# Performance work log

Measured on AMD Instinct MI355X. Metric: run time of the kernel, lower is better.

Reference implementation:

```python
import jax, jax.numpy as jnp
import numpy as np


def setup_inputs() -> dict:
    key = jax.random.key(0)
    k1, k2, k3 = jax.random.split(key, 3)
    B, F0, D = 8192, 39, 16
    L = 128
    hash_x = jax.random.normal(k1, (B, F0, D), dtype=jnp.float32)
    W0 = jax.random.normal(k2, (F0 * F0, L), dtype=jnp.float32) * 0.05
    W1 = jax.random.normal(k3, (F0 * (L // 2), L), dtype=jnp.float32) * 0.05
    return {"hash_x": hash_x, "W0": W0, "W1": W1}


def reference(hash_x, W0, W1):
    # CIN (Compressed Interaction Network) with layer sizes [128, 128], no bias.
    x0 = hash_x                      # [B, F0, D]
    B, F0, D = x0.shape
    L = W0.shape[1]                  # 128

    # --- layer 0 ---
    # outer product over fields per embedding dim: [B, D, F0, F0] -> flatten (i,j) row-major
    z0 = jnp.einsum('bid,bjd->bdij', x0, x0).reshape(B, D, F0 * F0)
    # conv1d with kernel width 1 == matmul over flattened field-pair dim
    cur0 = jax.nn.relu(jnp.einsum('bdk,kl->bld', z0, W0))   # [B, L, D]
    next_h, direct0 = jnp.split(cur0, 2, axis=1)            # each [B, L/2, D]

    # --- layer 1 (final) ---
    Fk = next_h.shape[1]                                     # L/2 = 64
    z1 = jnp.einsum('bid,bjd->bdij', x0, next_h).reshape(B, D, F0 * Fk)
    cur1 = jax.nn.relu(jnp.einsum('bdk,kl->bld', z1, W1))   # [B, L, D]

    result = jnp.concatenate([direct0, cur1], axis=1)        # [B, L/2 + L, D]
    return jnp.sum(result, axis=-1)                          # [B, 192]
```

## Files before the change

kernel.cpp:

```cpp
#include <hip/hip_runtime.h>
#include <hip/hip_bf16.h>


using short8 = __attribute__((ext_vector_type(8))) short;
using f32x16 = __attribute__((ext_vector_type(16))) float;

#define VSTR 52
#define V_BYTES (128 * VSTR * 4)
#define HSTR 72
#define H_BYTES (128 * HSTR * 2)
#define SMEM_BYTES (V_BYTES + H_BYTES)

#define NSL0 120
#define NSL1 156
#define NSL  (NSL0 + NSL1)
#define NFRAG (NSL * 4 * 64)

__device__ __forceinline__ unsigned short f2bf(float x) {
  __hip_bfloat16 h = __float2bfloat16(x);
  return __builtin_bit_cast(unsigned short, h);
}
__device__ __forceinline__ unsigned cvt2(float lo, float hi) {
  unsigned r;
  asm("v_cvt_pk_bf16_f32 %0, %1, %2" : "=v"(r) : "v"(lo), "v"(hi));
  return r;
}
__device__ __forceinline__ float bf_lo(unsigned w) {
  return __builtin_bit_cast(float, w << 16);
}
__device__ __forceinline__ float bf_hi(unsigned w) {
  return __builtin_bit_cast(float, w & 0xffff0000u);
}

__global__ void pack_w(const float* __restrict__ W0, const float* __restrict__ W1,
                       short8* __restrict__ wpk) {
  int fid = blockIdx.x * 256 + threadIdx.x;
  if (fid >= NFRAG) return;
  int lane = fid & 63;
  int t2 = fid >> 6;
  int nb = t2 & 3, s = t2 >> 2;
  int n = nb * 32 + (lane & 31);
  int kb = (lane >> 5) * 8;
  short8 frag;
  #pragma unroll
  for (int ii = 0; ii < 8; ii++) {
    float val;
    if (s < NSL0) {
      int k = s * 16 + kb + ii;
      int i = k / 48, j = k - i * 48;
      val = (i < 39 && j < 39) ? W0[(i * 39 + j) * 128 + n] : 0.f;
    } else {
      int k = (s - NSL0) * 16 + kb + ii;
      int i = k >> 6, j = k & 63;
      val = W1[(i * 64 + j) * 128 + n];
    }
    frag[ii] = (short)f2bf(val);
  }
  wpk[fid] = frag;
}

__global__ __launch_bounds__(256, 3) void cin_main(const float* __restrict__ X,
                                                   const short8* __restrict__ wpk,
                                                   float* __restrict__ out) {
  extern __shared__ char smem[];
  float* V          = (float*)smem;
  unsigned short* H = (unsigned short*)(smem + V_BYTES);

  const int t    = threadIdx.x;
  const int lane = t & 63;
  const int w    = t >> 6;
  const int l31  = lane & 31, hi = lane >> 5;
  const int b0   = blockIdx.x * 8;

  const float* xb = X + (size_t)b0 * 624;
  for (int f = t * 4; f < 4992; f += 1024) {
    float4 v4 = *(const float4*)(xb + f);
    int bl = f / 624;
    int rem = f - bl * 624;
    int i = rem >> 4, d0 = rem & 15;
    int r = bl * 16 + d0;
    V[(r + 0) * VSTR + i] = v4.x;
    V[(r + 1) * VSTR + i] = v4.y;
    V[(r + 2) * VSTR + i] = v4.z;
    V[(r + 3) * VSTR + i] = v4.w;
  }
  if (t < 128) {
    #pragma unroll
    for (int c = 39; c < VSTR; c++) V[t * VSTR + c] = 0.f;
  }
  __syncthreads();

  const int row = w * 32 + l31;
  const float* vr          = V + row * VSTR;
  const unsigned short* hr = H + row * HSTR;

  f32x16 acc[4];
  #pragma unroll
  for (int nb = 0; nb < 4; nb++)
    #pragma unroll
    for (int e = 0; e < 16; e++) acc[nb][e] = 0.f;

  short8 bc[4], bn[4];
  #pragma unroll
  for (int nb = 0; nb < 4; nb++) bn[nb] = wpk[nb * 64 + lane];

  #pragma unroll 1
  for (int i40 = 0; i40 < 40; i40++) {
    float vi = vr[i40];
    #pragma unroll
    for (int rr = 0; rr < 3; rr++) {
      int sg = i40 * 3 + rr;
      #pragma unroll
      for (int nb = 0; nb < 4; nb++) {
        bc[nb] = bn[nb];
        bn[nb] = wpk[(sg + 1) * 256 + nb * 64 + lane];
      }
      const float* jp = vr + 16 * rr + 8 * hi;
      float4 lo = *(const float4*)jp;
      float4 h4 = *(const float4*)(jp + 4);
      uint4 pk;
      pk.x = cvt2(vi * lo.x, vi * lo.y);
      pk.y = cvt2(vi * lo.z, vi * lo.w);
      pk.z = cvt2(vi * h4.x, vi * h4.y);
      pk.w = cvt2(vi * h4.z, vi * h4.w);
      short8 a = __builtin_bit_cast(short8, pk);
      #pragma unroll
      for (int nb = 0; nb < 4; nb++)
        acc[nb] = __builtin_amdgcn_mfma_f32_32x32x16_bf16(a, bc[nb], acc[nb], 0, 0, 0);
    }
  }

  #pragma unroll
  for (int nb = 0; nb < 2; nb++)
    #pragma unroll
    for (int r = 0; r < 16; r++) {
      int rt = (r & 3) + 8 * (r >> 2) + 4 * hi;
      H[(w * 32 + rt) * HSTR + nb * 32 + l31] = f2bf(fmaxf(acc[nb][r], 0.f));
    }
  #pragma unroll
  for (int nb = 2; nb < 4; nb++) {
    float s0 = 0.f, s1 = 0.f;
    #pragma unroll
    for (int r = 0; r < 8; r++)  s0 += fmaxf(acc[nb][r], 0.f);
    #pragma unroll
    for (int r = 8; r < 16; r++) s1 += fmaxf(acc[nb][r], 0.f);
    s0 += __shfl_xor(s0, 32);
    s1 += __shfl_xor(s1, 32);
    out[(size_t)(b0 + 2 * w + hi) * 192 + (nb - 2) * 32 + l31] = hi ? s1 : s0;
  }
  __syncthreads();

  #pragma unroll
  for (int nb = 0; nb < 4; nb++)
    #pragma unroll
    for (int e = 0; e < 16; e++) acc[nb][e] = 0.f;

  #pragma unroll 1
  for (int i39 = 0; i39 < 39; i39++) {
    float vi = vr[i39];
    #pragma unroll
    for (int rr = 0; rr < 4; rr++) {
      int sg = NSL0 + i39 * 4 + rr;
      #pragma unroll
      for (int nb = 0; nb < 4; nb++) {
        bc[nb] = bn[nb];
        if (sg + 1 < NSL) bn[nb] = wpk[(sg + 1) * 256 + nb * 64 + lane];
      }
      const unsigned short* jp = hr + 16 * rr + 8 * hi;
      uint4 hw = *(const uint4*)jp;
      uint4 pk;
      pk.x = cvt2(vi * bf_lo(hw.x), vi * bf_hi(hw.x));
      pk.y = cvt2(vi * bf_lo(hw.y), vi * bf_hi(hw.y));
      pk.z = cvt2(vi * bf_lo(hw.z), vi * bf_hi(hw.z));
      pk.w = cvt2(vi * bf_lo(hw.w), vi * bf_hi(hw.w));
      short8 a = __builtin_bit_cast(short8, pk);
      #pragma unroll
      for (int nb = 0; nb < 4; nb++)
        acc[nb] = __builtin_amdgcn_mfma_f32_32x32x16_bf16(a, bc[nb], acc[nb], 0, 0, 0);
    }
  }

  #pragma unroll
  for (int nb = 0; nb < 4; nb++) {
    float s0 = 0.f, s1 = 0.f;
    #pragma unroll
    for (int r = 0; r < 8; r++)  s0 += fmaxf(acc[nb][r], 0.f);
    #pragma unroll
    for (int r = 8; r < 16; r++) s1 += fmaxf(acc[nb][r], 0.f);
    s0 += __shfl_xor(s0, 32);
    s1 += __shfl_xor(s1, 32);
    out[(size_t)(b0 + 2 * w + hi) * 192 + 64 + nb * 32 + l31] = hi ? s1 : s0;
  }
}

extern "C" void kernel_launch(void* const* d_in, const int* in_sizes, int n_in,
                              void* d_out, int out_size, void* d_ws, size_t ws_size,
                              hipStream_t stream) {
  (void)in_sizes; (void)n_in; (void)out_size; (void)ws_size;
  const float* X  = (const float*)d_in[0];
  const float* W0 = (const float*)d_in[1];
  const float* W1 = (const float*)d_in[2];
  float* out = (float*)d_out;
  short8* wpk = (short8*)d_ws;

  pack_w<<<(NFRAG + 255) / 256, 256, 0, stream>>>(W0, W1, wpk);
  cin_main<<<1024, 256, SMEM_BYTES, stream>>>(X, wpk, out);
}
```

Before: 231.1 us.

## Double M-tile per wave and stage weight fragments through LDS with async loads

Each block now handles 16 batch items instead of 8, so every wave computes two 32-row M tiles that share each B fragment. The wave count fetching weights from global memory per output row drops by half. Weight fragments are loaded into double-buffered LDS with global_load_lds, which adds a barrier and a vmcnt wait on every k-step. X is now held in LDS as bf16, and the A operands for each row are preloaded into registers. In exchange the kernel uses more registers, runs at lower occupancy (launch bounds 2) with half as many blocks, and pays a per-step __syncthreads that may serialize the MFMA pipeline.

```diff
diff --git a/kernel.cpp b/kernel.cpp
--- a/kernel.cpp
+++ b/kernel.cpp
@@ -5,16 +5,17 @@
 using short8 = __attribute__((ext_vector_type(8))) short;
 using f32x16 = __attribute__((ext_vector_type(16))) float;
 
-#define VSTR 52
-#define V_BYTES (128 * VSTR * 4)
-#define HSTR 72
-#define H_BYTES (128 * HSTR * 2)
-#define SMEM_BYTES (V_BYTES + H_BYTES)
+#define VS 56
+#define V_BYTES (256 * VS * 2)
+#define HS 72
+#define H_BYTES (256 * HS * 2)
+#define BB_OFF (V_BYTES + H_BYTES)
+#define SMEM_BYTES (BB_OFF + 8192)
 
 #define NSL0 120
 #define NSL1 156
 #define NSL  (NSL0 + NSL1)
-#define NFRAG (NSL * 4 * 64)
+#define NFRAG (NSL * 256)
 
 __device__ __forceinline__ unsigned short f2bf(float x) {
   __hip_bfloat16 h = __float2bfloat16(x);
@@ -30,6 +31,21 @@
 }
 __device__ __forceinline__ float bf_hi(unsigned w) {
   return __builtin_bit_cast(float, w & 0xffff0000u);
+}
+__device__ __forceinline__ float bf2f(unsigned short b) {
+  return __builtin_bit_cast(float, ((unsigned)b) << 16);
+}
+__device__ __forceinline__ short8 mk_a(float vi, uint4 p) {
+  uint4 pk;
+  pk.x = cvt2(vi * bf_lo(p.x), vi * bf_hi(p.x));
+  pk.y = cvt2(vi * bf_lo(p.y), vi * bf_hi(p.y));
+  pk.z = cvt2(vi * bf_lo(p.z), vi * bf_hi(p.z));
+  pk.w = cvt2(vi * bf_lo(p.w), vi * bf_hi(p.w));
+  return __builtin_bit_cast(short8, pk);
+}
+__device__ __forceinline__ void stage16(const void* g, char* l) {
+  __builtin_amdgcn_global_load_lds((const __attribute__((address_space(1))) void*)g,
+                                   (__attribute__((address_space(3))) void*)l, 16, 0, 0);
 }
 
 __global__ void pack_w(const float* __restrict__ W0, const float* __restrict__ W1,
@@ -59,138 +75,168 @@
   wpk[fid] = frag;
 }
 
-__global__ __launch_bounds__(256, 3) void cin_main(const float* __restrict__ X,
+__global__ __launch_bounds__(256, 2) void cin_main(const float* __restrict__ X,
                                                    const short8* __restrict__ wpk,
                                                    float* __restrict__ out) {
   extern __shared__ char smem[];
-  float* V          = (float*)smem;
-  unsigned short* H = (unsigned short*)(smem + V_BYTES);
+  unsigned short* Vb = (unsigned short*)smem;
+  unsigned short* H  = (unsigned short*)(smem + V_BYTES);
+  char* Bsm          = smem + BB_OFF;
 
   const int t    = threadIdx.x;
   const int lane = t & 63;
   const int w    = t >> 6;
   const int l31  = lane & 31, hi = lane >> 5;
-  const int b0   = blockIdx.x * 8;
+  const int b0   = blockIdx.x * 16;
 
   const float* xb = X + (size_t)b0 * 624;
-  for (int f = t * 4; f < 4992; f += 1024) {
+  for (int f = t * 4; f < 9984; f += 1024) {
     float4 v4 = *(const float4*)(xb + f);
     int bl = f / 624;
     int rem = f - bl * 624;
     int i = rem >> 4, d0 = rem & 15;
     int r = bl * 16 + d0;
-    V[(r + 0) * VSTR + i] = v4.x;
-    V[(r + 1) * VSTR + i] = v4.y;
-    V[(r + 2) * VSTR + i] = v4.z;
-    V[(r + 3) * VSTR + i] = v4.w;
-  }
-  if (t < 128) {
-    #pragma unroll
-    for (int c = 39; c < VSTR; c++) V[t * VSTR + c] = 0.f;
-  }
+    Vb[(r + 0) * VS + i] = f2bf(v4.x);
+    Vb[(r + 1) * VS + i] = f2bf(v4.y);
+    Vb[(r + 2) * VS + i] = f2bf(v4.z);
+    Vb[(r + 3) * VS + i] = f2bf(v4.w);
+  }
+  #pragma unroll
+  for (int c = 39; c < VS; c++) Vb[t * VS + c] = 0;
+
+  stage16((const char*)wpk + ((size_t)0 * 256 + w * 64 + lane) * 16, Bsm + (w << 10));
+  asm volatile("s_waitcnt vmcnt(0)" ::: "memory");
   __syncthreads();
 
-  const int row = w * 32 + l31;
-  const float* vr          = V + row * VSTR;
-  const unsigned short* hr = H + row * HSTR;
-
-  f32x16 acc[4];
-  #pragma unroll
-  for (int nb = 0; nb < 4; nb++)
-    #pragma unroll
-    for (int e = 0; e < 16; e++) acc[nb][e] = 0.f;
-
-  short8 bc[4], bn[4];
-  #pragma unroll
-  for (int nb = 0; nb < 4; nb++) bn[nb] = wpk[nb * 64 + lane];
-
+  const int row0 = w * 64 + l31;
+  const int row1 = row0 + 32;
+
+  uint4 vp0[3], vp1[3];
+  #pragma unroll
+  for (int rr = 0; rr < 3; rr++) {
+    vp0[rr] = *(const uint4*)(Vb + row0 * VS + 16 * rr + 8 * hi);
+    vp1[rr] = *(const uint4*)(Vb + row1 * VS + 16 * rr + 8 * hi);
+  }
+
+  f32x16 acc[2][4];
+  #pragma unroll
+  for (int mi = 0; mi < 2; mi++)
+    #pragma unroll
+    for (int nb = 0; nb < 4; nb++)
+      #pragma unroll
+      for (int e = 0; e < 16; e++) acc[mi][nb][e] = 0.f;
+
+  int sg = 0;
   #pragma unroll 1
-  for (int i40 = 0; i40 < 40; i40++) {
-    float vi = vr[i40];
+  for (int ig = 0; ig < 40; ig++) {
+    float vi0 = bf2f(Vb[row0 * VS + ig]);
+    float vi1 = bf2f(Vb[row1 * VS + ig]);
     #pragma unroll
     for (int rr = 0; rr < 3; rr++) {
-      int sg = i40 * 3 + rr;
-      #pragma unroll
-      for (int nb = 0; nb < 4; nb++) {
-        bc[nb] = bn[nb];
-        bn[nb] = wpk[(sg + 1) * 256 + nb * 64 + lane];
+      stage16((const char*)wpk + ((size_t)(sg + 1) * 256 + w * 64 + lane) * 16,
+              Bsm + (((sg + 1) & 1) << 12) + (w << 10));
+      const char* bb = Bsm + ((sg & 1) << 12) + (lane << 4);
+      short8 bf0 = *(const short8*)(bb + 0);
+      short8 bf1 = *(const short8*)(bb + 1024);
+      short8 bf2 = *(const short8*)(bb + 2048);
+      short8 bf3 = *(const short8*)(bb + 3072);
+      short8 a0 = mk_a(vi0, vp0[rr]);
+      short8 a1 = mk_a(vi1, vp1[rr]);
+      acc[0][0] = __builtin_amdgcn_mfma_f32_32x32x16_bf16(a0, bf0, acc[0][0], 0, 0, 0);
+      acc[1][0] = __builtin_amdgcn_mfma_f32_32x32x16_bf16(a1, bf0, acc[1][0], 0, 0, 0);
+      acc[0][1] = __builtin_amdgcn_mfma_f32_32x32x16_bf16(a0, bf1, acc[0][1], 0, 0, 0);
+      acc[1][1] = __builtin_amdgcn_mfma_f32_32x32x16_bf16(a1, bf1, acc[1][1], 0, 0, 0);
+      acc[0][2] = __builtin_amdgcn_mfma_f32_32x32x16_bf16(a0, bf2, acc[0][2], 0, 0, 0);
+      acc[1][2] = __builtin_amdgcn_mfma_f32_32x32x16_bf16(a1, bf2, acc[1][2], 0, 0, 0);
+      acc[0][3] = __builtin_amdgcn_mfma_f32_32x32x16_bf16(a0, bf3, acc[0][3], 0, 0, 0);
+      acc[1][3] = __builtin_amdgcn_mfma_f32_32x32x16_bf16(a1, bf3, acc[1][3], 0, 0, 0);
+      asm volatile("s_waitcnt vmcnt(0)" ::: "memory");
+      __syncthreads();
+      sg++;
+    }
+  }
+
+  #pragma unroll
+  for (int mi = 0; mi < 2; mi++)
+    #pragma unroll
+    for (int nb = 0; nb < 2; nb++)
+      #pragma unroll
+      for (int r = 0; r < 16; r++) {
+        int rt = (r & 3) + 8 * (r >> 2) + 4 * hi;
+        H[(w * 64 + mi * 32 + rt) * HS + nb * 32 + l31] = f2bf(fmaxf(acc[mi][nb][r], 0.f));
       }
-      const float* jp = vr + 16 * rr + 8 * hi;
-      float4 lo = *(const float4*)jp;
-      float4 h4 = *(const float4*)(jp + 4);
-      uint4 pk;
-      pk.x = cvt2(vi * lo.x, vi * lo.y);
-      pk.y = cvt2(vi * lo.z, vi * lo.w);
-      pk.z = cvt2(vi * h4.x, vi * h4.y);
-      pk.w = cvt2(vi * h4.z, vi * h4.w);
-      short8 a = __builtin_bit_cast(short8, pk);
-      #pragma unroll
-      for (int nb = 0; nb < 4; nb++)
-        acc[nb] = __builtin_amdgcn_mfma_f32_32x32x16_bf16(a, bc[nb], acc[nb], 0, 0, 0);
-    }
-  }
-
-  #pragma unroll
-  for (int nb = 0; nb < 2; nb++)
-    #pragma unroll
-    for (int r = 0; r < 16; r++) {
-      int rt = (r & 3) + 8 * (r >> 2) + 4 * hi;
-      H[(w * 32 + rt) * HSTR + nb * 32 + l31] = f2bf(fmaxf(acc[nb][r], 0.f));
-    }
-  #pragma unroll
-  for (int nb = 2; nb < 4; nb++) {
-    float s0 = 0.f, s1 = 0.f;
-    #pragma unroll
-    for (int r = 0; r < 8; r++)  s0 += fmaxf(acc[nb][r], 0.f);
-    #pragma unroll
-    for (int r = 8; r < 16; r++) s1 += fmaxf(acc[nb][r], 0.f);
-    s0 += __shfl_xor(s0, 32);
-    s1 += __shfl_xor(s1, 32);
-    out[(size_t)(b0 + 2 * w + hi) * 192 + (nb - 2) * 32 + l31] = hi ? s1 : s0;
-  }
+  #pragma unroll
+  for (int mi = 0; mi < 2; mi++)
+    #pragma unroll
+    for (int nb = 2; nb < 4; nb++) {
+      float s0 = 0.f, s1 = 0.f;
+      #pragma unroll
+      for (int r = 0; r < 8; r++)  s0 += fmaxf(acc[mi][nb][r], 0.f);
+      #pragma unroll
+      for (int r = 8; r < 16; r++) s1 += fmaxf(acc[mi][nb][r], 0.f);
+      s0 += __shfl_xor(s0, 32);
+      s1 += __shfl_xor(s1, 32);
+      out[(size_t)(b0 + 4 * w + 2 * mi + hi) * 192 + (nb - 2) * 32 + l31] = hi ? s1 : s0;
+    }
   __syncthreads();
 
-  #pragma unroll
-  for (int nb = 0; nb < 4; nb++)
-    #pragma unroll
-    for (int e = 0; e < 16; e++) acc[nb][e] = 0.f;
+  uint4 hp0[4], hp1[4];
+  #pragma unroll
+  for (int rr = 0; rr < 4; rr++) {
+    hp0[rr] = *(const uint4*)(H + row0 * HS + 16 * rr + 8 * hi);
+    hp1[rr] = *(const uint4*)(H + row1 * HS + 16 * rr + 8 * hi);
+  }
+
+  #pragma unroll
+  for (int mi = 0; mi < 2; mi++)
+    #pragma unroll
+    for (int nb = 0; nb < 4; nb++)
+      #pragma unroll
+      for (int e = 0; e < 16; e++) acc[mi][nb][e] = 0.f;
 
   #pragma unroll 1
-  for (int i39 = 0; i39 < 39; i39++) {
-    float vi = vr[i39];
+  for (int ig = 0; ig < 39; ig++) {
+    float vi0 = bf2f(Vb[row0 * VS + ig]);
+    float vi1 = bf2f(Vb[row1 * VS + ig]);
     #pragma unroll
     for (int rr = 0; rr < 4; rr++) {
-      int sg = NSL0 + i39 * 4 + rr;
-      #pragma unroll
-      for (int nb = 0; nb < 4; nb++) {
-        bc[nb] = bn[nb];
-        if (sg + 1 < NSL) bn[nb] = wpk[(sg + 1) * 256 + nb * 64 + lane];
-      }
-      const unsigned short* jp = hr + 16 * rr + 8 * hi;
-      uint4 hw = *(const uint4*)jp;
-      uint4 pk;
-      pk.x = cvt2(vi * bf_lo(hw.x), vi * bf_hi(hw.x));
-      pk.y = cvt2(vi * bf_lo(hw.y), vi * bf_hi(hw.y));
-      pk.z = cvt2(vi * bf_lo(hw.z), vi * bf_hi(hw.z));
-      pk.w = cvt2(vi * bf_lo(hw.w), vi * bf_hi(hw.w));
-      short8 a = __builtin_bit_cast(short8, pk);
-      #pragma unroll
-      for (int nb = 0; nb < 4; nb++)
-        acc[nb] = __builtin_amdgcn_mfma_f32_32x32x16_bf16(a, bc[nb], acc[nb], 0, 0, 0);
-    }
-  }
-
-  #pragma unroll
-  for (int nb = 0; nb < 4; nb++) {
-    float s0 = 0.f, s1 = 0.f;
-    #pragma unroll
-    for (int r = 0; r < 8; r++)  s0 += fmaxf(acc[nb][r], 0.f);
-    #pragma unroll
-    for (int r = 8; r < 16; r++) s1 += fmaxf(acc[nb][r], 0.f);
-    s0 += __shfl_xor(s0, 32);
-    s1 += __shfl_xor(s1, 32);
-    out[(size_t)(b0 + 2 * w + hi) * 192 + 64 + nb * 32 + l31] = hi ? s1 : s0;
-  }
+      if (sg + 1 < NSL)
+        stage16((const char*)wpk + ((size_t)(sg + 1) * 256 + w * 64 + lane) * 16,
+                Bsm + (((sg + 1) & 1) << 12) + (w << 10));
+      const char* bb = Bsm + ((sg & 1) << 12) + (lane << 4);
+      short8 bf0 = *(const short8*)(bb + 0);
+      short8 bf1 = *(const short8*)(bb + 1024);
+      short8 bf2 = *(const short8*)(bb + 2048);
+      short8 bf3 = *(const short8*)(bb + 3072);
+      short8 a0 = mk_a(vi0, hp0[rr]);
+      short8 a1 = mk_a(vi1, hp1[rr]);
+      acc[0][0] = __builtin_amdgcn_mfma_f32_32x32x16_bf16(a0, bf0, acc[0][0], 0, 0, 0);
+      acc[1][0] = __builtin_amdgcn_mfma_f32_32x32x16_bf16(a1, bf0, acc[1][0], 0, 0, 0);
+      acc[0][1] = __builtin_amdgcn_mfma_f32_32x32x16_bf16(a0, bf1, acc[0][1], 0, 0, 0);
+      acc[1][1] = __builtin_amdgcn_mfma_f32_32x32x16_bf16(a1, bf1, acc[1][1], 0, 0, 0);
+      acc[0][2] = __builtin_amdgcn_mfma_f32_32x32x16_bf16(a0, bf2, acc[0][2], 0, 0, 0);
+      acc[1][2] = __builtin_amdgcn_mfma_f32_32x32x16_bf16(a1, bf2, acc[1][2], 0, 0, 0);
+      acc[0][3] = __builtin_amdgcn_mfma_f32_32x32x16_bf16(a0, bf3, acc[0][3], 0, 0, 0);
+      acc[1][3] = __builtin_amdgcn_mfma_f32_32x32x16_bf16(a1, bf3, acc[1][3], 0, 0, 0);
+      asm volatile("s_waitcnt vmcnt(0)" ::: "memory");
+      __syncthreads();
+      sg++;
+    }
+  }
+
+  #pragma unroll
+  for (int mi = 0; mi < 2; mi++)
+    #pragma unroll
+    for (int nb = 0; nb < 4; nb++) {
+      float s0 = 0.f, s1 = 0.f;
+      #pragma unroll
+      for (int r = 0; r < 8; r++)  s0 += fmaxf(acc[mi][nb][r], 0.f);
+      #pragma unroll
+      for (int r = 8; r < 16; r++) s1 += fmaxf(acc[mi][nb][r], 0.f);
+      s0 += __shfl_xor(s0, 32);
+      s1 += __shfl_xor(s1, 32);
+      out[(size_t)(b0 + 4 * w + 2 * mi + hi) * 192 + 64 + nb * 32 + l31] = hi ? s1 : s0;
+    }
 }
 
 extern "C" void kernel_launch(void* const* d_in, const int* in_sizes, int n_in,
@@ -203,6 +249,9 @@
   float* out = (float*)d_out;
   short8* wpk = (short8*)d_ws;
 
+  (void)hipFuncSetAttribute((const void*)cin_main,
+                            hipFuncAttributeMaxDynamicSharedMemorySize, SMEM_BYTES);
+
   pack_w<<<(NFRAG + 255) / 256, 256, 0, stream>>>(W0, W1, wpk);
-  cin_main<<<1024, 256, SMEM_BYTES, stream>>>(X, wpk, out);
-}
+  cin_main<<<512, 256, SMEM_BYTES, stream>>>(X, wpk, out);
+}
```

Result: faster. 188.4 us (-18.5%).
